# Performance work log

Hardware: AMD Instinct MI355X
Metric: run time of the kernel (lower is better)

The kernel has to match this reference:

```python
import jax, jax.numpy as jnp
import numpy as np

B, T, HID = 4, 2048, 2048
NH = 16
HD = HID // NH  # 128
THETA = 10000.0


def _rope_cache(seq_len, head_dim):
    half = head_dim // 2
    freqs = 1.0 / THETA ** (jnp.arange(half, dtype=jnp.float32) / half)
    pos = jnp.arange(seq_len, dtype=jnp.float32)
    angles = pos[:, None] * freqs[None, :]  # [T, hd/2]
    return jnp.cos(angles), jnp.sin(angles)


def _apply_rope(x, cos, sin):
    # x: [B, nh, T, hd]; cos/sin: [T, hd/2]
    x_even, x_odd = x[..., 0::2], x[..., 1::2]
    c = cos[None, None, :, :]
    s = sin[None, None, :, :]
    rot_even = x_even * c - x_odd * s
    rot_odd = x_even * s + x_odd * c
    # interleave back: stack on new last axis then flatten
    return jnp.stack([rot_even, rot_odd], axis=-1).reshape(x.shape)


def setup_inputs() -> dict:
    key = jax.random.key(0)
    k1, k2, k3, k4 = jax.random.split(key, 4)
    x = jax.random.normal(k1, (B, T, HID), dtype=jnp.float32)
    w_qkv = jax.random.normal(k2, (3 * HID, HID), dtype=jnp.float32) * 0.02
    w_proj = jax.random.normal(k3, (HID, HID), dtype=jnp.float32) * 0.02
    b_proj = jax.random.normal(k4, (HID,), dtype=jnp.float32) * 0.02
    cos, sin = _rope_cache(T, HD)
    return {"x": x, "w_qkv": w_qkv, "w_proj": w_proj, "b_proj": b_proj,
            "cos": cos, "sin": sin}


def reference(x, w_qkv, w_proj, b_proj, cos, sin):
    Bx, Tx, Hx = x.shape
    qkv = jnp.einsum('bth,oh->bto', x, w_qkv)  # [B,T,3H]
    qkv = qkv.reshape(Bx, Tx, 3, NH, HD)
    q = jnp.transpose(qkv[:, :, 0], (0, 2, 1, 3))  # [B,nh,T,hd]
    k = jnp.transpose(qkv[:, :, 1], (0, 2, 1, 3))
    v = jnp.transpose(qkv[:, :, 2], (0, 2, 1, 3))
    q = _apply_rope(q, cos, sin)
    k = _apply_rope(k, cos, sin)
    scale = 1.0 / np.sqrt(HD).astype(np.float32)
    scores = jnp.einsum('bhqd,bhkd->bhqk', q, k) * scale  # [B,nh,T,T]
    attn = jax.nn.softmax(scores, axis=-1)
    out = jnp.einsum('bhqk,bhkd->bhqd', attn, v)  # [B,nh,T,hd]
    out = jnp.transpose(out, (0, 2, 1, 3)).reshape(Bx, Tx, Hx)
    return jnp.einsum('bth,oh->bto', out, w_proj) + b_proj
```

## Files before the change

### kernel.cpp

```cpp
#include <hip/hip_runtime.h>
#include <stdint.h>


typedef unsigned short u16;
typedef unsigned int   u32;
typedef unsigned long long u64;
typedef __attribute__((ext_vector_type(8))) short short8;
typedef __attribute__((ext_vector_type(4))) float f32x4;

__device__ __forceinline__ void gload16(const void* g, void* l) {
  __builtin_amdgcn_global_load_lds((const __attribute__((address_space(1))) void*)g,
                                   (__attribute__((address_space(3))) void*)l, 16, 0, 0);
}

__device__ __forceinline__ u16 f2bf(float f) {
  u32 u = __builtin_bit_cast(u32, f);
  u32 r = (u + 0x7fffu + ((u >> 16) & 1u)) >> 16;
  return (u16)r;
}
__device__ __forceinline__ float bf2f(u16 b) {
  u32 u = ((u32)b) << 16;
  return __builtin_bit_cast(float, u);
}

__global__ __launch_bounds__(256) void cvt_kernel(const float* __restrict__ src,
                                                  u16* __restrict__ dst) {
  size_t i = ((size_t)blockIdx.x * 256 + threadIdx.x) * 4;
  f32x4 v = *(const f32x4*)(src + i);
  u64 pk = (u64)f2bf(v[0]) | ((u64)f2bf(v[1]) << 16) |
           ((u64)f2bf(v[2]) << 32) | ((u64)f2bf(v[3]) << 48);
  *(u64*)(dst + i) = pk;
}

template <int MODE>
__global__ __launch_bounds__(256, 2) void gemm_bt(const u16* __restrict__ A,
                                                  const u16* __restrict__ B,
                                                  void* __restrict__ C,
                                                  int M, int N, int K,
                                                  const float* __restrict__ bias) {
  __shared__ __attribute__((aligned(16))) u16 As[128 * 32];
  __shared__ __attribute__((aligned(16))) u16 Bs[128 * 32];
  const int tid  = threadIdx.x;
  const int wave = tid >> 6, lane = tid & 63;
  const int quad = lane >> 4, l16 = lane & 15;
  const int m0 = blockIdx.y * 128, n0 = blockIdx.x * 128;
  const int wr = wave >> 1, wc = wave & 1;
  const int lrow = lane >> 2;
  const int lcol = (lane & 3) * 8;
  f32x4 acc[4][4] = {};

  const size_t Abase = (size_t)(m0 + wave * 32 + lrow) * K + lcol;
  const size_t Bbase = (size_t)(n0 + wave * 32 + lrow) * K + lcol;

  for (int k0 = 0; k0 < K; k0 += 32) {
    gload16(A + Abase + k0,                 &As[(wave * 32) * 32]);
    gload16(A + Abase + (size_t)16 * K + k0, &As[(wave * 32 + 16) * 32]);
    gload16(B + Bbase + k0,                 &Bs[(wave * 32) * 32]);
    gload16(B + Bbase + (size_t)16 * K + k0, &Bs[(wave * 32 + 16) * 32]);
    __syncthreads();
    short8 a[4], b[4];
#pragma unroll
    for (int rt = 0; rt < 4; rt++)
      a[rt] = *(const short8*)&As[(wr * 64 + rt * 16 + l16) * 32 + quad * 8];
#pragma unroll
    for (int ct = 0; ct < 4; ct++)
      b[ct] = *(const short8*)&Bs[(wc * 64 + ct * 16 + l16) * 32 + quad * 8];
#pragma unroll
    for (int rt = 0; rt < 4; rt++)
#pragma unroll
      for (int ct = 0; ct < 4; ct++)
        acc[rt][ct] = __builtin_amdgcn_mfma_f32_16x16x32_bf16(a[rt], b[ct], acc[rt][ct], 0, 0, 0);
    __syncthreads();
  }
#pragma unroll
  for (int rt = 0; rt < 4; rt++) {
#pragma unroll
    for (int ct = 0; ct < 4; ct++) {
      const int col = n0 + wc * 64 + ct * 16 + l16;
      float bv = (MODE == 1) ? bias[col] : 0.0f;
#pragma unroll
      for (int r = 0; r < 4; r++) {
        const int row = m0 + wr * 64 + rt * 16 + quad * 4 + r;
        if (MODE == 0)
          ((u16*)C)[(size_t)row * N + col] = f2bf(acc[rt][ct][r]);
        else
          ((float*)C)[(size_t)row * N + col] = acc[rt][ct][r] + bv;
      }
    }
  }
}

__global__ __launch_bounds__(256) void rope_reshape(const u16* __restrict__ qkv,
                                                    const float* __restrict__ cosb,
                                                    const float* __restrict__ sinb,
                                                    u16* __restrict__ Qr,
                                                    u16* __restrict__ Kr,
                                                    u16* __restrict__ Vt) {
  __shared__ __attribute__((aligned(16))) u16 Vl[32 * 132];
  const int tb = blockIdx.x;
  const int bh = blockIdx.y;
  const int tid = threadIdx.x;
  const int b = bh >> 4, h = bh & 15;
  const float scale = 0.08838834764831845f;
#pragma unroll
  for (int p8 = 0; p8 < 8; p8++) {
    int p = p8 * 256 + tid;
    int r = p >> 6, i = p & 63;
    int t = tb * 32 + r;
    size_t base = (size_t)(b * 2048 + t) * 6144 + h * 128 + 2 * i;
    float c = cosb[t * 64 + i], s = sinb[t * 64 + i];
    u32 q2 = *(const u32*)(qkv + base);
    float qe = bf2f((u16)q2), qo = bf2f((u16)(q2 >> 16));
    u32 qw = (u32)f2bf((qe * c - qo * s) * scale) | ((u32)f2bf((qe * s + qo * c) * scale) << 16);
    *(u32*)(Qr + ((size_t)bh * 2048 + t) * 128 + 2 * i) = qw;
    u32 k2 = *(const u32*)(qkv + base + 2048);
    float ke = bf2f((u16)k2), ko = bf2f((u16)(k2 >> 16));
    u32 kw = (u32)f2bf(ke * c - ko * s) | ((u32)f2bf(ke * s + ko * c) << 16);
    *(u32*)(Kr + ((size_t)bh * 2048 + t) * 128 + 2 * i) = kw;
    u32 v2 = *(const u32*)(qkv + base + 4096);
    *(u32*)&Vl[r * 132 + 2 * i] = v2;
  }
  __syncthreads();
#pragma unroll
  for (int u8 = 0; u8 < 8; u8++) {
    int u = u8 * 256 + tid;
    int d = u >> 4, tp = (u & 15) * 2;
    u32 lo = Vl[tp * 132 + d];
    u32 hi = Vl[(tp + 1) * 132 + d];
    *(u32*)(Vt + ((size_t)bh * 128 + d) * 2048 + tb * 32 + tp) = lo | (hi << 16);
  }
}

__global__ __launch_bounds__(256, 2) void flash_attn(const u16* __restrict__ Q,
                                                     const u16* __restrict__ K,
                                                     const u16* __restrict__ Vt,
                                                     u16* __restrict__ Out) {
  __shared__ __attribute__((aligned(16))) u16 Klds[32 * 512];
  __shared__ __attribute__((aligned(16))) u16 Vlds[32 * 512];
  const int qb = blockIdx.x;
  const int bh = blockIdx.y;
  const int tid = threadIdx.x;
  const int wave = tid >> 6, lane = tid & 63;
  const int quad = lane >> 4, l16 = lane & 15;
  const int lrow4 = lane >> 2, lcol8 = (lane & 3) * 8;
  const u16* Qh = Q + (size_t)bh * 2048 * 128;
  const u16* Kh = K + (size_t)bh * 2048 * 128;
  const u16* Vh = Vt + (size_t)bh * 128 * 2048;

  short8 qf[2][4];
#pragma unroll
  for (int rt = 0; rt < 2; rt++)
#pragma unroll
    for (int kk = 0; kk < 4; kk++)
      qf[rt][kk] = *(const short8*)(Qh + (size_t)(qb * 128 + wave * 32 + rt * 16 + l16) * 128 + kk * 32 + quad * 8);

  f32x4 o[2][8] = {};
  float mrow[2][4], lrowv[2][4];
#pragma unroll
  for (int rt = 0; rt < 2; rt++)
#pragma unroll
    for (int r = 0; r < 4; r++) { mrow[rt][r] = -1e30f; lrowv[rt][r] = 0.f; }

  for (int kb = 0; kb < 16; kb++) {
    __syncthreads();
#pragma unroll
    for (int c = 0; c < 8; c++) {
      int ch = wave * 8 + c;
      int tbb = ch >> 2, kk = ch & 3;
      gload16(Kh + (size_t)(kb * 128 + tbb * 16 + lrow4) * 128 + kk * 32 + lcol8, &Klds[ch * 512]);
      gload16(Vh + (size_t)(tbb * 16 + lrow4) * 2048 + kb * 128 + kk * 32 + lcol8, &Vlds[ch * 512]);
    }
    __syncthreads();

    f32x4 s[2][8];
#pragma unroll
    for (int nt = 0; nt < 8; nt++) {
      short8 kf[4];
#pragma unroll
      for (int kk = 0; kk < 4; kk++)
        kf[kk] = *(const short8*)&Klds[(nt * 4 + kk) * 512 + l16 * 32 + quad * 8];
#pragma unroll
      for (int rt = 0; rt < 2; rt++) {
        f32x4 a = {};
#pragma unroll
        for (int kk = 0; kk < 4; kk++)
          a = __builtin_amdgcn_mfma_f32_16x16x32_bf16(qf[rt][kk], kf[kk], a, 0, 0, 0);
        s[rt][nt] = a;
      }
    }

#pragma unroll
    for (int rt = 0; rt < 2; rt++)
#pragma unroll
      for (int r = 0; r < 4; r++) {
        float mx = s[rt][0][r];
#pragma unroll
        for (int nt = 1; nt < 8; nt++) mx = fmaxf(mx, s[rt][nt][r]);
        mx = fmaxf(mx, __shfl_xor(mx, 1));
        mx = fmaxf(mx, __shfl_xor(mx, 2));
        mx = fmaxf(mx, __shfl_xor(mx, 4));
        mx = fmaxf(mx, __shfl_xor(mx, 8));
        float mnew = fmaxf(mrow[rt][r], mx);
        float alpha = __expf(mrow[rt][r] - mnew);
        mrow[rt][r] = mnew;
        float sum = 0.f;
#pragma unroll
        for (int nt = 0; nt < 8; nt++) {
          float p = __expf(s[rt][nt][r] - mnew);
          s[rt][nt][r] = p;
          sum += p;
        }
        sum += __shfl_xor(sum, 1);
        sum += __shfl_xor(sum, 2);
        sum += __shfl_xor(sum, 4);
        sum += __shfl_xor(sum, 8);
        lrowv[rt][r] = lrowv[rt][r] * alpha + sum;
#pragma unroll
        for (int dt = 0; dt < 8; dt++) o[rt][dt][r] *= alpha;
      }

    __syncthreads();
    u16* P = &Klds[wave * 4096];
#pragma unroll
    for (int rt = 0; rt < 2; rt++)
#pragma unroll
      for (int nt = 0; nt < 8; nt++)
#pragma unroll
        for (int r = 0; r < 4; r++)
          P[(rt * 16 + quad * 4 + r) * 128 + nt * 16 + l16] = f2bf(s[rt][nt][r]);
    __syncthreads();

#pragma unroll
    for (int kk = 0; kk < 4; kk++) {
      short8 pf[2];
#pragma unroll
      for (int rt = 0; rt < 2; rt++)
        pf[rt] = *(const short8*)&P[(rt * 16 + l16) * 128 + kk * 32 + quad * 8];
#pragma unroll
      for (int dt = 0; dt < 8; dt++) {
        short8 vf = *(const short8*)&Vlds[(dt * 4 + kk) * 512 + l16 * 32 + quad * 8];
#pragma unroll
        for (int rt = 0; rt < 2; rt++)
          o[rt][dt] = __builtin_amdgcn_mfma_f32_16x16x32_bf16(pf[rt], vf, o[rt][dt], 0, 0, 0);
      }
    }
  }

  const int b = bh >> 4, h = bh & 15;
#pragma unroll
  for (int rt = 0; rt < 2; rt++) {
    float inv[4];
#pragma unroll
    for (int r = 0; r < 4; r++) inv[r] = 1.0f / lrowv[rt][r];
#pragma unroll
    for (int dt = 0; dt < 8; dt++) {
      int d = dt * 16 + l16;
#pragma unroll
      for (int r = 0; r < 4; r++) {
        int t = qb * 128 + wave * 32 + rt * 16 + quad * 4 + r;
        Out[((size_t)(b * 2048 + t)) * 2048 + h * 128 + d] = f2bf(o[rt][dt][r] * inv[r]);
      }
    }
  }
}

extern "C" void kernel_launch(void* const* d_in, const int* in_sizes, int n_in,
                              void* d_out, int out_size, void* d_ws, size_t ws_size,
                              hipStream_t stream) {
  const float* x      = (const float*)d_in[0];
  const float* w_qkv  = (const float*)d_in[1];
  const float* w_proj = (const float*)d_in[2];
  const float* b_proj = (const float*)d_in[3];
  const float* cosb   = (const float*)d_in[4];
  const float* sinb   = (const float*)d_in[5];
  char* ws = (char*)d_ws;
  const size_t MB = 1024 * 1024;
  u16* xb   = (u16*)(ws + 0);
  u16* Qr   = (u16*)(ws + 0);
  u16* wqb  = (u16*)(ws + 32 * MB);
  u16* Kr   = (u16*)(ws + 32 * MB);
  u16* qkv  = (u16*)(ws + 64 * MB);
  u16* attn = (u16*)(ws + 64 * MB);
  u16* Vt   = (u16*)(ws + 160 * MB);
  u16* wpb  = (u16*)(ws + 192 * MB);

  cvt_kernel<<<16384, 256, 0, stream>>>(x, xb);
  cvt_kernel<<<12288, 256, 0, stream>>>(w_qkv, wqb);
  cvt_kernel<<<4096, 256, 0, stream>>>(w_proj, wpb);

  gemm_bt<0><<<dim3(48, 64), 256, 0, stream>>>(xb, wqb, qkv, 8192, 6144, 2048, nullptr);
  rope_reshape<<<dim3(64, 64), 256, 0, stream>>>(qkv, cosb, sinb, Qr, Kr, Vt);
  flash_attn<<<dim3(16, 64), 256, 0, stream>>>(Qr, Kr, Vt, attn);
  gemm_bt<1><<<dim3(16, 64), 256, 0, stream>>>(attn, wpb, (float*)d_out, 8192, 2048, 2048, b_proj);
}
```

Baseline: 758.9 us.

## Use XOR-swizzled row-major LDS layout for K/V/P and drop P barrier

Changes the K and V shared-memory tiles from a chunked layout to row-major rows of 256 bytes with an XOR swizzle, applied on both the global-to-LDS loads and the fragment reads. The aim is to cut LDS bank conflicts. The P staging buffer uses the same swizzle, and the block-wide barrier between writing P and reading it is replaced by a wave-local lgkmcnt wait, since each wave reads only its own P region. Raises wave priority around the MFMA loops with s_setprio. The risk is that the swizzle arithmetic must exactly match the lane-to-address pattern of global_load_lds.

```diff
diff --git a/kernel.cpp b/kernel.cpp
--- a/kernel.cpp
+++ b/kernel.cpp
@@ -135,17 +135,20 @@
                                                      const u16* __restrict__ K,
                                                      const u16* __restrict__ Vt,
                                                      u16* __restrict__ Out) {
-  __shared__ __attribute__((aligned(16))) u16 Klds[32 * 512];
-  __shared__ __attribute__((aligned(16))) u16 Vlds[32 * 512];
+  __shared__ __attribute__((aligned(16))) u16 Klds[128 * 128];
+  __shared__ __attribute__((aligned(16))) u16 Vlds[128 * 128];
   const int qb = blockIdx.x;
   const int bh = blockIdx.y;
   const int tid = threadIdx.x;
   const int wave = tid >> 6, lane = tid & 63;
   const int quad = lane >> 4, l16 = lane & 15;
-  const int lrow4 = lane >> 2, lcol8 = (lane & 3) * 8;
   const u16* Qh = Q + (size_t)bh * 2048 * 128;
   const u16* Kh = K + (size_t)bh * 2048 * 128;
   const u16* Vh = Vt + (size_t)bh * 128 * 2048;
+  char* Kc = (char*)Klds;
+  char* Vc = (char*)Vlds;
+  char* Pc = Kc + wave * 8192;
+  const int swz = (l16 & 7) << 4;
 
   short8 qf[2][4];
 #pragma unroll
@@ -164,21 +167,22 @@
   for (int kb = 0; kb < 16; kb++) {
     __syncthreads();
 #pragma unroll
-    for (int c = 0; c < 8; c++) {
-      int ch = wave * 8 + c;
-      int tbb = ch >> 2, kk = ch & 3;
-      gload16(Kh + (size_t)(kb * 128 + tbb * 16 + lrow4) * 128 + kk * 32 + lcol8, &Klds[ch * 512]);
-      gload16(Vh + (size_t)(tbb * 16 + lrow4) * 2048 + kb * 128 + kk * 32 + lcol8, &Vlds[ch * 512]);
+    for (int i = 0; i < 8; i++) {
+      int row = wave * 32 + i * 4 + quad;
+      int colel = (l16 * 8) ^ ((row & 7) * 8);
+      gload16(Kh + (size_t)(kb * 128 + row) * 128 + colel, Kc + (wave * 32 + i * 4) * 256);
+      gload16(Vh + (size_t)row * 2048 + kb * 128 + colel,  Vc + (wave * 32 + i * 4) * 256);
     }
     __syncthreads();
 
     f32x4 s[2][8];
+    __builtin_amdgcn_s_setprio(1);
 #pragma unroll
     for (int nt = 0; nt < 8; nt++) {
       short8 kf[4];
 #pragma unroll
       for (int kk = 0; kk < 4; kk++)
-        kf[kk] = *(const short8*)&Klds[(nt * 4 + kk) * 512 + l16 * 32 + quad * 8];
+        kf[kk] = *(const short8*)(Kc + ((nt * 16 + l16) << 8) + ((kk * 64 + quad * 16) ^ swz));
 #pragma unroll
       for (int rt = 0; rt < 2; rt++) {
         f32x4 a = {};
@@ -188,6 +192,7 @@
         s[rt][nt] = a;
       }
     }
+    __builtin_amdgcn_s_setprio(0);
 
 #pragma unroll
     for (int rt = 0; rt < 2; rt++)
@@ -220,30 +225,34 @@
       }
 
     __syncthreads();
-    u16* P = &Klds[wave * 4096];
 #pragma unroll
     for (int rt = 0; rt < 2; rt++)
 #pragma unroll
       for (int nt = 0; nt < 8; nt++)
 #pragma unroll
-        for (int r = 0; r < 4; r++)
-          P[(rt * 16 + quad * 4 + r) * 128 + nt * 16 + l16] = f2bf(s[rt][nt][r]);
-    __syncthreads();
-
+        for (int r = 0; r < 4; r++) {
+          int rp = rt * 16 + quad * 4 + r;
+          *(u16*)(Pc + (rp << 8) + ((nt * 32 + l16 * 2) ^ ((rp & 7) << 4))) = f2bf(s[rt][nt][r]);
+        }
+    asm volatile("s_waitcnt lgkmcnt(0)" ::: "memory");
+    __builtin_amdgcn_sched_barrier(0);
+
+    __builtin_amdgcn_s_setprio(1);
 #pragma unroll
     for (int kk = 0; kk < 4; kk++) {
       short8 pf[2];
 #pragma unroll
       for (int rt = 0; rt < 2; rt++)
-        pf[rt] = *(const short8*)&P[(rt * 16 + l16) * 128 + kk * 32 + quad * 8];
+        pf[rt] = *(const short8*)(Pc + ((rt * 16 + l16) << 8) + ((kk * 64 + quad * 16) ^ swz));
 #pragma unroll
       for (int dt = 0; dt < 8; dt++) {
-        short8 vf = *(const short8*)&Vlds[(dt * 4 + kk) * 512 + l16 * 32 + quad * 8];
+        short8 vf = *(const short8*)(Vc + ((dt * 16 + l16) << 8) + ((kk * 64 + quad * 16) ^ swz));
 #pragma unroll
         for (int rt = 0; rt < 2; rt++)
           o[rt][dt] = __builtin_amdgcn_mfma_f32_16x16x32_bf16(pf[rt], vf, o[rt][dt], 0, 0, 0);
       }
     }
+    __builtin_amdgcn_s_setprio(0);
   }
 
   const int b = bh >> 4, h = bh & 15;
```

New measurement: 1.071 ms. 41.2% more time.
